# Kernel optimization log

Hardware: AMD Instinct MI355X
Metric: run time of the kernel (lower is better)

## Reference

```python
import jax, jax.numpy as jnp
import numpy as np
from jax import lax

CONV1_T = 15.0
CONV2_T = 10.0
K2 = 8
R2 = 1


def _conv2d(x, w):
    # F.conv2d, stride 1, no padding, no bias
    return lax.conv_general_dilated(x, w, (1, 1), 'VALID',
                                    dimension_numbers=('NCHW', 'OIHW', 'NCHW'))


def _pad(x, p):
    return jnp.pad(x, ((0, 0), (0, 0), (p, p), (p, p)))


def _fire(pot, thr):
    # sf.fire: threshold_(pot, thr, 0) (strictly greater), spikes = sign
    pot_t = jnp.where(pot > thr, pot, jnp.zeros((), pot.dtype))
    return jnp.sign(pot_t), pot_t


def _max_pool(x, k, s):
    return lax.reduce_window(x, jnp.array(-jnp.inf, x.dtype), lax.max,
                             (1, 1, k, k), (1, 1, s, s), 'VALID')


def _pointwise_inhibition(pot):
    # sf.pointwise_inhibition: keep, at each (h,w), only the feature that spikes
    # earliest (ties broken by max potential); zero it entirely if nothing fired.
    T, C, H, W = pot.shape
    max_vals = pot.max(axis=1)                      # [T,H,W]
    max_idx = pot.argmax(axis=1)                    # [T,H,W] winning feature per t
    clamp = jnp.sign(max_vals)                      # [T,H,W] did any feature spike at t
    earliest = jnp.clip((T - clamp.sum(axis=0)).astype(jnp.int32), 0, T - 1)  # [H,W]
    win_feat = jnp.take_along_axis(max_idx, earliest[None].astype(max_idx.dtype), axis=0)[0]  # [H,W]
    fired_last = clamp[-1]                          # [H,W] any spike by final step
    rows = jnp.arange(H)[:, None]
    cols = jnp.arange(W)[None, :]
    coef = jnp.zeros((C, H, W), pot.dtype).at[win_feat, rows, cols].set(fired_last)
    return pot * coef[None]


def _get_k_winners(pot, spk, kwta, r):
    # sf.get_k_winners: rank neurons by (earliness, potential), iterative argmax
    # with per-feature and spatial-radius inhibition (NMS-like).
    T, C, H, W = pot.shape
    earliest = jnp.clip((T - spk.sum(axis=0)).astype(jnp.int32), 0, T - 1)  # [C,H,W]
    values = jnp.take_along_axis(pot, earliest[None], axis=0)[0]            # [C,H,W]
    trunc = spk * values[None]
    v = trunc.max() * T
    trunc = trunc + spk * v
    total = trunc.sum(axis=0)                                               # [C,H,W]

    def step(tot, _):
        flat = tot.reshape(-1)
        idx = jnp.argmax(flat).astype(jnp.int32)
        mval = flat[idx]
        c = idx // (H * W)
        rem = idx % (H * W)
        row = rem // W
        col = rem % W
        fmask = (jnp.arange(C) == c)[:, None, None]
        rmask = (jnp.abs(jnp.arange(H) - row) <= r)[None, :, None]
        cmask = (jnp.abs(jnp.arange(W) - col) <= r)[None, None, :]
        tot = jnp.where(fmask | (rmask & cmask), jnp.zeros((), tot.dtype), tot)
        winner = jnp.where(mval > 0, jnp.stack([c, row, col]),
                           jnp.full((3,), -1, jnp.int32))
        return tot, winner

    _, winners = lax.scan(step, total, None, length=kwta)
    return winners  # [kwta, 3] = (feature, row, col), -1 padded


def setup_inputs():
    key = jax.random.key(0)
    k1, k2, k3 = jax.random.split(key, 3)
    # cumulative spike-wave input [T=15, C=6, H=252, W=252]
    inp = jax.random.randint(k1, (15, 6, 252, 252), 0, 2, dtype=jnp.int32)
    # snn.Convolution weights ~ N(mean=0.8, std=0.05)
    w1 = 0.8 + 0.05 * jax.random.normal(k2, (30, 6, 5, 5), dtype=jnp.float32)
    w2 = 0.8 + 0.05 * jax.random.normal(k3, (250, 30, 3, 3), dtype=jnp.float32)
    return {"input": inp, "max_layer": 2, "w1": w1, "w2": w2}


def reference(input, max_layer, w1, w2):
    # training path, max_layer == 2
    x = _pad(input.astype(jnp.float32), 2)        # [15,6,256,256]
    pot = _conv2d(x, w1)                          # [15,30,252,252]
    spk, pot = _fire(pot, CONV1_T)
    spk_in = _pad(_max_pool(spk, 2, 2), 1)        # [15,30,128,128]
    pot = _conv2d(spk_in, w2)                     # [15,250,126,126]
    spk, pot = _fire(pot, CONV2_T)
    pot = _pointwise_inhibition(pot)
    spk = jnp.sign(pot)
    winners = _get_k_winners(pot, spk, K2, R2)
    return spk, pot, winners
```

## Files before the change

### kernel.cpp

```cpp
#include <hip/hip_runtime.h>
#include <limits.h>

#define T_STEPS 15
#define CIN     6
#define HIN     252
#define C1      30
#define SH      128
#define SW      128
#define C2      250
#define NPIX    15876
#define NTP     (T_STEPS*NPIX)
#define THR1    15.0f
#define THR2    10.0f
#define KWTA    8
#define SPK_ELEMS  59535000L

__global__ __launch_bounds__(256) void consts_k(
    const float* __restrict__ w2, float* __restrict__ wT,
    float* __restrict__ Sthr, float* __restrict__ consts) {
  const int f = threadIdx.x;
  if (blockIdx.x < 270) {
    int k = blockIdx.x;
    wT[k * 256 + f] = (f < C2) ? w2[(long)f * 270 + k] : 0.f;
    return;
  }
  __shared__ float sS[256];
  float S = 0.f;
  if (f < C2) {
    const float* wf = w2 + (long)f * 270;
    for (int k = 0; k < 270; ++k) S = fmaf(wf[k], 1.0f, S);
  }
  float st = (f < C2 && S > THR2) ? S : 0.f;
  Sthr[f] = st;
  sS[f] = (f < C2) ? st : -1.f;
  __syncthreads();
  if (f == 0) {
    float bv = -1.f; int bf = 0;
    for (int i = 0; i < C2; ++i) { if (sS[i] > bv) { bv = sS[i]; bf = i; } }
    consts[0] = bv;
    ((int*)consts)[1] = bf;
  }
}

#define G1 5
__global__ __launch_bounds__(128, 6) void conv1_v4b(
    const int* __restrict__ inp, const float* __restrict__ w1,
    float* __restrict__ spk_in, unsigned long long* __restrict__ bitm) {
  __shared__ float srow[6][256];
  __shared__ unsigned long long s_bal[2][G1];
  const int ph = blockIdx.x;
  const int cg = blockIdx.y;
  const int t  = blockIdx.z;
  const int pw = threadIdx.x;

  float acc[G1][4];
  #pragma unroll
  for (int cc = 0; cc < G1; ++cc) {
    acc[cc][0] = 0.f; acc[cc][1] = 0.f; acc[cc][2] = 0.f; acc[cc][3] = 0.f;
  }

  for (int ic = 0; ic < CIN; ++ic) {
    __syncthreads();
    for (int i = pw; i < 6 * 256; i += 128) {
      int rr = i >> 8, col = i & 255;
      int row = 2 * ph - 2 + rr, in_col = col - 2;
      float v = 0.f;
      if (row >= 0 && row < HIN && in_col >= 0 && in_col < HIN)
        v = (float)inp[((long)(t * CIN + ic) * HIN + row) * HIN + in_col];
      srow[rr][col] = v;
    }
    __syncthreads();

    #pragma unroll
    for (int rr = 0; rr < 6; ++rr) {
      float row6[6];
      #pragma unroll
      for (int j = 0; j < 6; ++j)
        row6[j] = srow[rr][(2 * pw + j) & 255];
      #pragma unroll
      for (int cc = 0; cc < G1; ++cc) {
        const int c = cg * G1 + cc;
        const float* wp = w1 + ((c * CIN) + ic) * 25;
        if (rr < 5) {
          #pragma unroll
          for (int kw = 0; kw < 5; ++kw) {
            float wv = wp[rr * 5 + kw];
            acc[cc][0] = fmaf(wv, row6[kw],     acc[cc][0]);
            acc[cc][1] = fmaf(wv, row6[kw + 1], acc[cc][1]);
          }
        }
        if (rr >= 1) {
          #pragma unroll
          for (int kw = 0; kw < 5; ++kw) {
            float wv = wp[(rr - 1) * 5 + kw];
            acc[cc][2] = fmaf(wv, row6[kw],     acc[cc][2]);
            acc[cc][3] = fmaf(wv, row6[kw + 1], acc[cc][3]);
          }
        }
      }
    }
  }
  unsigned fbits = 0;
  #pragma unroll
  for (int cc = 0; cc < G1; ++cc) {
    bool fired = (pw < 126) && (acc[cc][0] > THR1 || acc[cc][1] > THR1 ||
                                acc[cc][2] > THR1 || acc[cc][3] > THR1);
    if (fired) fbits |= 1u << cc;
    if (pw < 126) {
      int c = cg * G1 + cc;
      spk_in[((long)(t * C1 + c) * SH + (ph + 1)) * SW + (pw + 1)] = fired ? 1.f : 0.f;
    }
  }
  #pragma unroll
  for (int cc = 0; cc < G1; ++cc) {
    unsigned long long b = __ballot((fbits >> cc) & 1);
    if ((pw & 63) == 0) s_bal[pw >> 6][cc] = b;
  }
  __syncthreads();
  if (pw < G1) {
    unsigned long long b0 = s_bal[0][pw], b1 = s_bal[1][pw];
    unsigned long long w0 = b0 << 1;
    unsigned long long w1 = (b1 << 1) | (b0 >> 63);
    int c = cg * G1 + pw;
    unsigned long long* bp = bitm + 2 * (((long)(t * C1 + c)) * SH + (ph + 1));
    bp[0] = w0; bp[1] = w1;
  }
}

__global__ __launch_bounds__(128) void classify2(
    const unsigned long long* __restrict__ bitm, const float* __restrict__ consts,
    float* __restrict__ meta_val, int* __restrict__ meta_f,
    unsigned char* __restrict__ allones) {
  const int oh = blockIdx.x, t = blockIdx.y, ow = threadIdx.x;
  unsigned long long lo = ~0ull, hi = ~0ull;
  for (int c = 0; c < C1; ++c) {
    const unsigned long long* bp = bitm + 2 * (((long)(t * C1 + c)) * SH + oh);
    lo &= bp[0] & bp[2] & bp[4];
    hi &= bp[1] & bp[3] & bp[5];
  }
  if (ow >= 126) return;
  unsigned long long x = (ow < 64)
      ? ((lo >> ow) | (ow ? (hi << (64 - ow)) : 0ull))
      : (hi >> (ow - 64));
  bool ao = (x & 7ull) == 7ull;
  int tp = t * NPIX + oh * 126 + ow;
  allones[tp] = ao ? 1 : 0;
  if (ao) { meta_val[tp] = consts[0]; meta_f[tp] = ((const int*)consts)[1]; }
}

__global__ __launch_bounds__(256) void dense_meta(
    const float* __restrict__ spk_in, const float* __restrict__ wT,
    const unsigned char* __restrict__ allones,
    float* __restrict__ meta_val, int* __restrict__ meta_f) {
  __shared__ int s_list[256];
  __shared__ int s_cnt;
  __shared__ float s_win[270][8];
  __shared__ unsigned long long s_part[4];
  const int tid = threadIdx.x;
  if (tid == 0) s_cnt = 0;
  __syncthreads();
  {
    int i = blockIdx.x + tid * 1024;
    if (i < NTP && !allones[i]) { int pos = atomicAdd(&s_cnt, 1); s_list[pos] = i; }
  }
  __syncthreads();
  const int cnt = s_cnt;
  for (int g = 0; g < cnt; g += 8) {
    int m = cnt - g; if (m > 8) m = 8;
    for (int j = tid; j < 270 * 8; j += 256) {
      int k = j >> 3, q = j & 7;
      float v = 0.f;
      if (q < m) {
        int tp = s_list[g + q];
        int t = tp / NPIX, p = tp % NPIX;
        int oh = p / 126, ow = p % 126;
        int c = k / 9, kh = (k % 9) / 3, kw = k % 3;
        v = spk_in[((long)(t * C1 + c) * SH + oh + kh) * SW + ow + kw];
      }
      s_win[k][q] = v;
    }
    __syncthreads();
    float acc[8];
    #pragma unroll
    for (int q = 0; q < 8; ++q) acc[q] = 0.f;
    for (int k = 0; k < 270; ++k) {
      float wv = wT[k * 256 + tid];
      #pragma unroll
      for (int q = 0; q < 8; ++q)
        acc[q] = fmaf(wv, s_win[k][q], acc[q]);
    }
    #pragma unroll
    for (int q = 0; q < 8; ++q) {
      unsigned long long key = 0;
      if (tid < C2) {
        float v = acc[q] > THR2 ? acc[q] : 0.f;
        key = ((unsigned long long)__float_as_uint(v) << 8) | (unsigned)(255 - tid);
      }
      #pragma unroll
      for (int s = 1; s < 64; s <<= 1) {
        unsigned long long o = __shfl_xor(key, s, 64);
        if (o > key) key = o;
      }
      if ((tid & 63) == 0) s_part[tid >> 6] = key;
      __syncthreads();
      if (tid == 0 && q < m) {
        unsigned long long k0 = s_part[0];
        if (s_part[1] > k0) k0 = s_part[1];
        if (s_part[2] > k0) k0 = s_part[2];
        if (s_part[3] > k0) k0 = s_part[3];
        int tp = s_list[g + q];
        meta_val[tp] = __uint_as_float((unsigned)(k0 >> 8));
        meta_f[tp] = 255 - (int)(k0 & 255);
      }
      __syncthreads();
    }
  }
}

__global__ __launch_bounds__(256) void inhibit2(
    const float* __restrict__ meta_val, const int* __restrict__ meta_f,
    int* __restrict__ winfeat) {
  int p = blockIdx.x * 256 + threadIdx.x;
  if (p >= NPIX) return;
  int n = 0; bool last = false;
  #pragma unroll
  for (int t = 0; t < T_STEPS; ++t) {
    bool fr = meta_val[t * NPIX + p] > 0.f;
    n += fr ? 1 : 0;
    if (t == T_STEPS - 1) last = fr;
  }
  int e = T_STEPS - n;
  if (e > T_STEPS - 1) e = T_STEPS - 1;
  if (e < 0) e = 0;
  winfeat[p] = last ? meta_f[e * NPIX + p] : -1;
}

__global__ __launch_bounds__(256) void winner_pv(
    const int* __restrict__ winfeat, const unsigned char* __restrict__ allones,
    const float* __restrict__ Sthr, const float* __restrict__ spk_in,
    const float* __restrict__ w2, float* __restrict__ spk_out,
    float* __restrict__ pot_out, float* __restrict__ pvbuf) {
  int tp = blockIdx.x * 256 + threadIdx.x;
  if (tp >= NTP) return;
  int t = tp / NPIX, p = tp % NPIX;
  int w = winfeat[p];
  if (w < 0) { pvbuf[tp] = 0.f; return; }
  float pt;
  if (allones[tp]) {
    pt = Sthr[w];
  } else {
    int oh = p / 126, ow = p % 126;
    const float* wb = w2 + (long)w * 270;
    float a = 0.f;
    for (int c = 0; c < C1; ++c) {
      const float* sb = spk_in + ((long)(t * C1 + c) * SH + oh) * SW + ow;
      #pragma unroll
      for (int kh = 0; kh < 3; ++kh)
        #pragma unroll
        for (int kw = 0; kw < 3; ++kw)
          a = fmaf(wb[c * 9 + kh * 3 + kw], sb[kh * SW + kw], a);
    }
    pt = a > THR2 ? a : 0.f;
  }
  pvbuf[tp] = pt;
  long o = ((long)t * C2 + w) * NPIX + p;
  pot_out[o] = pt;
  spk_out[o] = pt > 0.f ? 1.f : 0.f;
}

__global__ __launch_bounds__(256) void cand_k(
    const int* __restrict__ winfeat, const float* __restrict__ pvbuf,
    float* __restrict__ cand_val, int* __restrict__ cand_n) {
  int p = blockIdx.x * 256 + threadIdx.x;
  if (p >= NPIX) return;
  int w = winfeat[p];
  if (w < 0) { cand_val[p] = 0.f; cand_n[p] = 0; return; }
  float pv[T_STEPS]; int n = 0;
  #pragma unroll
  for (int t = 0; t < T_STEPS; ++t) {
    float v = pvbuf[t * NPIX + p];
    pv[t] = v;
    n += v > 0.f ? 1 : 0;
  }
  int e = T_STEPS - n; if (e > 14) e = 14; if (e < 0) e = 0;
  float cv = 0.f;
  #pragma unroll
  for (int t = 0; t < T_STEPS; ++t) if (t == e) cv = pv[t];
  cand_val[p] = cv;
  cand_n[p] = n;
}

__global__ __launch_bounds__(1024) void kwin_select2(
    const float* __restrict__ cand_val, const int* __restrict__ cand_n,
    const int* __restrict__ winfeat, float* __restrict__ winners_out) {
  __shared__ float s_tot[NPIX];
  __shared__ unsigned char s_w[NPIX];
  __shared__ unsigned char s_rem[NPIX];
  __shared__ unsigned char s_fr[256];
  __shared__ unsigned long long s_part[16];
  __shared__ float s_max[16];
  __shared__ int s_sel;
  const int tid = threadIdx.x;
  const int wid = tid >> 6, lane = tid & 63;

  if (tid < 256) s_fr[tid] = 0;

  float m = 0.f;
  for (int p = tid; p < NPIX; p += 1024) {
    int w = winfeat[p];
    s_w[p] = (w < 0) ? 255 : (unsigned char)w;
    s_rem[p] = 0;
    float cv = cand_val[p];
    s_tot[p] = cv;
    m = fmaxf(m, cv);
  }
  #pragma unroll
  for (int s = 1; s < 64; s <<= 1) m = fmaxf(m, __shfl_xor(m, s, 64));
  if (lane == 0) s_max[wid] = m;
  __syncthreads();
  if (tid == 0) {
    float mm = s_max[0];
    for (int i = 1; i < 16; ++i) mm = fmaxf(mm, s_max[i]);
    s_max[0] = mm * (float)T_STEPS;
  }
  __syncthreads();
  const float v = s_max[0];
  for (int p = tid; p < NPIX; p += 1024) {
    float x = s_tot[p] + v;
    int n = cand_n[p];
    float tot = 0.f;
    for (int q = 0; q < n; ++q) tot += x;
    s_tot[p] = tot;
  }
  __syncthreads();

  for (int round = 0; round < KWTA; ++round) {
    unsigned long long best = 0;
    for (int p = tid; p < NPIX; p += 1024) {
      unsigned char w = s_w[p];
      if (w == 255 || s_rem[p] || s_fr[w]) continue;
      unsigned long long flat = (unsigned long long)w * NPIX + (unsigned)p;
      unsigned long long key =
          ((unsigned long long)__float_as_uint(s_tot[p]) << 25) | (0x1FFFFFFull - flat);
      if (key > best) best = key;
    }
    #pragma unroll
    for (int s = 1; s < 64; s <<= 1) {
      unsigned long long o = __shfl_xor(best, s, 64);
      if (o > best) best = o;
    }
    if (lane == 0) s_part[wid] = best;
    __syncthreads();
    if (tid == 0) {
      unsigned long long b = s_part[0];
      for (int i = 1; i < 16; ++i) if (s_part[i] > b) b = s_part[i];
      float tot = __uint_as_float((unsigned)(b >> 25));
      if (b != 0 && tot > 0.f) {
        int flat = (int)(0x1FFFFFFull - (b & 0x1FFFFFFull));
        int c = flat / NPIX, p = flat % NPIX;
        winners_out[round * 3 + 0] = (float)c;
        winners_out[round * 3 + 1] = (float)(p / 126);
        winners_out[round * 3 + 2] = (float)(p % 126);
        s_fr[c] = 1;
        s_sel = p;
      } else {
        winners_out[round * 3 + 0] = -1.f;
        winners_out[round * 3 + 1] = -1.f;
        winners_out[round * 3 + 2] = -1.f;
        s_sel = -1;
      }
    }
    __syncthreads();
    int sel = s_sel;
    if (sel >= 0) {
      int rw = sel / 126, cw = sel % 126;
      for (int p = tid; p < NPIX; p += 1024) {
        int row = p / 126, col = p % 126;
        if (row >= rw - 1 && row <= rw + 1 && col >= cw - 1 && col <= cw + 1)
          s_rem[p] = 1;
      }
    }
    __syncthreads();
  }
}

extern "C" void kernel_launch(void* const* d_in, const int* in_sizes, int n_in,
                              void* d_out, int out_size, void* d_ws, size_t ws_size,
                              hipStream_t stream) {
  const int*   inp = (const int*)d_in[0];
  const float* w1  = (const float*)d_in[2];
  const float* w2  = (const float*)d_in[3];

  float* out = (float*)d_out;
  float* spk_out = out;
  float* pot_out = out + SPK_ELEMS;
  float* win_out = out + 2 * SPK_ELEMS;

  float* ws = (float*)d_ws;
  float* spk_in   = ws;
  float* meta_val = ws + 7372800;
  int*   meta_f   = (int*)ws + 7610940;
  int*   winfeat  = (int*)ws + 7849080;
  float* cand_val = ws + 7864956;
  int*   cand_n   = (int*)ws + 7880832;
  float* Sthr     = ws + 7896708;
  float* consts   = ws + 7896964;
  float* wT       = ws + 7896968;
  unsigned char* allones = (unsigned char*)(ws + 7966088);
  unsigned long long* bitm = (unsigned long long*)(ws + 8025624);

  hipMemsetAsync(spk_in, 0, 7372800 * sizeof(float), stream);
  hipMemsetAsync(bitm, 0, 115200 * sizeof(unsigned long long), stream);
  hipMemsetAsync(out, 0, 2 * SPK_ELEMS * sizeof(float), stream);

  consts_k<<<271, 256, 0, stream>>>(w2, wT, Sthr, consts);
  {
    dim3 g(126, 6, 15);
    conv1_v4b<<<g, 128, 0, stream>>>(inp, w1, spk_in, bitm);
  }
  {
    dim3 g(126, 15);
    classify2<<<g, 128, 0, stream>>>(bitm, consts, meta_val, meta_f, allones);
  }
  dense_meta<<<1024, 256, 0, stream>>>(spk_in, wT, allones, meta_val, meta_f);
  inhibit2<<<(NPIX + 255) / 256, 256, 0, stream>>>(meta_val, meta_f, winfeat);
  winner_pv<<<(NTP + 255) / 256, 256, 0, stream>>>(
      winfeat, allones, Sthr, spk_in, w2, spk_out, pot_out, meta_val );
  cand_k<<<(NPIX + 255) / 256, 256, 0, stream>>>(winfeat, meta_val, cand_val, cand_n);
  kwin_select2<<<1, 1024, 0, stream>>>(cand_val, cand_n, winfeat, win_out);
}
```

Before: 795.6 us.

## Double-buffer conv1 input rows and process two pooled rows per block

The conv1 kernel now uses 256-thread blocks that each compute two pooled output rows, sharing an 8-row input tile instead of two separate 6-row tiles. Input channel tiles are double-buffered in shared memory so the load of the next channel overlaps compute on the current one, which removes one barrier per channel. Each block stages less redundant data and the grid is halved, at the cost of more shared memory per block and a lower occupancy bound.

```diff
diff --git a/kernel.cpp b/kernel.cpp
--- a/kernel.cpp
+++ b/kernel.cpp
@@ -43,15 +43,19 @@
 }
 
 #define G1 5
-__global__ __launch_bounds__(128, 6) void conv1_v4b(
+__global__ __launch_bounds__(256, 4) void conv1_v5(
     const int* __restrict__ inp, const float* __restrict__ w1,
     float* __restrict__ spk_in, unsigned long long* __restrict__ bitm) {
-  __shared__ float srow[6][256];
-  __shared__ unsigned long long s_bal[2][G1];
-  const int ph = blockIdx.x;
+  __shared__ float srow[2][8][256];
+  __shared__ unsigned long long s_bal[4][G1];
+  const int bx = blockIdx.x;
   const int cg = blockIdx.y;
   const int t  = blockIdx.z;
-  const int pw = threadIdx.x;
+  const int tid = threadIdx.x;
+  const int gr = tid >> 7, pw = tid & 127;
+  const int rowbase = 4 * bx - 2;
+  const int in_col = tid - 2;
+  const bool colok = (in_col >= 0) && (in_col < HIN);
 
   float acc[G1][4];
   #pragma unroll
@@ -59,47 +63,62 @@
     acc[cc][0] = 0.f; acc[cc][1] = 0.f; acc[cc][2] = 0.f; acc[cc][3] = 0.f;
   }
 
+  {
+    const int* base = inp + ((long)(t * CIN + 0) * HIN) * HIN;
+    #pragma unroll
+    for (int j = 0; j < 8; ++j) {
+      int row = rowbase + j;
+      float v = 0.f;
+      if (row >= 0 && row < HIN && colok) v = (float)base[row * HIN + in_col];
+      srow[0][j][tid] = v;
+    }
+  }
+  __syncthreads();
+
   for (int ic = 0; ic < CIN; ++ic) {
-    __syncthreads();
-    for (int i = pw; i < 6 * 256; i += 128) {
-      int rr = i >> 8, col = i & 255;
-      int row = 2 * ph - 2 + rr, in_col = col - 2;
-      float v = 0.f;
-      if (row >= 0 && row < HIN && in_col >= 0 && in_col < HIN)
-        v = (float)inp[((long)(t * CIN + ic) * HIN + row) * HIN + in_col];
-      srow[rr][col] = v;
-    }
-    __syncthreads();
-
+    const int b = ic & 1;
+    if (ic < CIN - 1) {
+      const int* base = inp + ((long)(t * CIN + ic + 1) * HIN) * HIN;
+      #pragma unroll
+      for (int j = 0; j < 8; ++j) {
+        int row = rowbase + j;
+        float v = 0.f;
+        if (row >= 0 && row < HIN && colok) v = (float)base[row * HIN + in_col];
+        srow[b ^ 1][j][tid] = v;
+      }
+    }
     #pragma unroll
-    for (int rr = 0; rr < 6; ++rr) {
+    for (int r = 0; r < 6; ++r) {
       float row6[6];
       #pragma unroll
       for (int j = 0; j < 6; ++j)
-        row6[j] = srow[rr][(2 * pw + j) & 255];
+        row6[j] = srow[b][2 * gr + r][(2 * pw + j) & 255];
       #pragma unroll
       for (int cc = 0; cc < G1; ++cc) {
         const int c = cg * G1 + cc;
         const float* wp = w1 + ((c * CIN) + ic) * 25;
-        if (rr < 5) {
+        if (r < 5) {
           #pragma unroll
           for (int kw = 0; kw < 5; ++kw) {
-            float wv = wp[rr * 5 + kw];
+            float wv = wp[r * 5 + kw];
             acc[cc][0] = fmaf(wv, row6[kw],     acc[cc][0]);
             acc[cc][1] = fmaf(wv, row6[kw + 1], acc[cc][1]);
           }
         }
-        if (rr >= 1) {
+        if (r >= 1) {
           #pragma unroll
           for (int kw = 0; kw < 5; ++kw) {
-            float wv = wp[(rr - 1) * 5 + kw];
+            float wv = wp[(r - 1) * 5 + kw];
             acc[cc][2] = fmaf(wv, row6[kw],     acc[cc][2]);
             acc[cc][3] = fmaf(wv, row6[kw + 1], acc[cc][3]);
           }
         }
       }
     }
-  }
+    __syncthreads();
+  }
+
+  const int ph = 2 * bx + gr;
   unsigned fbits = 0;
   #pragma unroll
   for (int cc = 0; cc < G1; ++cc) {
@@ -113,16 +132,17 @@
   }
   #pragma unroll
   for (int cc = 0; cc < G1; ++cc) {
-    unsigned long long b = __ballot((fbits >> cc) & 1);
-    if ((pw & 63) == 0) s_bal[pw >> 6][cc] = b;
-  }
-  __syncthreads();
-  if (pw < G1) {
-    unsigned long long b0 = s_bal[0][pw], b1 = s_bal[1][pw];
+    unsigned long long bl = __ballot((fbits >> cc) & 1);
+    if ((tid & 63) == 0) s_bal[tid >> 6][cc] = bl;
+  }
+  __syncthreads();
+  if (tid < 2 * G1) {
+    int gr2 = tid / G1, cc = tid % G1;
+    unsigned long long b0 = s_bal[2 * gr2 + 0][cc], b1 = s_bal[2 * gr2 + 1][cc];
     unsigned long long w0 = b0 << 1;
     unsigned long long w1 = (b1 << 1) | (b0 >> 63);
-    int c = cg * G1 + pw;
-    unsigned long long* bp = bitm + 2 * (((long)(t * C1 + c)) * SH + (ph + 1));
+    int c = cg * G1 + cc;
+    unsigned long long* bp = bitm + 2 * (((long)(t * C1 + c)) * SH + (2 * bx + gr2 + 1));
     bp[0] = w0; bp[1] = w1;
   }
 }
@@ -415,8 +435,8 @@
 
   consts_k<<<271, 256, 0, stream>>>(w2, wT, Sthr, consts);
   {
-    dim3 g(126, 6, 15);
-    conv1_v4b<<<g, 128, 0, stream>>>(inp, w1, spk_in, bitm);
+    dim3 g(63, 6, 15);
+    conv1_v5<<<g, 256, 0, stream>>>(inp, w1, spk_in, bitm);
   }
   {
     dim3 g(126, 15);
```

Measured after the change: 767.8 us. 3.5% less time.
